# Kernel optimization log

Hardware: AMD Instinct MI355X
Metric: run time of the kernel (lower is better)

## Reference

```python
import jax, jax.numpy as jnp
import numpy as np

B, N, FIN, FOUT, E, R = 4, 8000, 256, 512, 640000, 44
NT = B * N
EPS = 1e-5


def setup_inputs() -> dict:
    key = jax.random.key(0)
    ks = jax.random.split(key, 10)
    s = 0.02
    return {
        "x": jax.random.normal(ks[0], (B, N, FIN), jnp.float32),
        "edge_index": jax.random.randint(ks[1], (2, E), 0, NT, jnp.int32),
        "edge_attr": jax.random.randint(ks[2], (E,), 0, R, jnp.int32),
        "gamma1": jnp.ones((FIN,), jnp.float32),
        "beta1": jnp.zeros((FIN,), jnp.float32),
        "W1": jax.random.normal(ks[3], (R, FIN, FOUT), jnp.float32) * s,
        "root1": jax.random.normal(ks[4], (FIN, FOUT), jnp.float32) * s,
        "b1": jnp.zeros((FOUT,), jnp.float32),
        "gamma2": jnp.ones((FOUT,), jnp.float32),
        "beta2": jnp.zeros((FOUT,), jnp.float32),
        "W2": jax.random.normal(ks[5], (R, FOUT, FOUT), jnp.float32) * s,
        "root2": jax.random.normal(ks[6], (FOUT, FOUT), jnp.float32) * s,
        "b2": jnp.zeros((FOUT,), jnp.float32),
        "Wskip": jax.random.normal(ks[7], (FIN, FOUT), jnp.float32) * s,
        "bskip": jnp.zeros((FOUT,), jnp.float32),
    }


def batchnorm(x, gamma, beta):
    # torch BatchNorm1d on (B, C, N) in training mode: stats over (B, N) per channel
    mu = jnp.mean(x, axis=(0, 1))
    var = jnp.var(x, axis=(0, 1))  # biased, matches torch normalization
    return (x - mu) * jax.lax.rsqrt(var + EPS) * gamma + beta


def rgcn_conv(h, src, dst, rel, W, root, bias):
    # out[i] = h[i]@root + bias + sum_r mean_{j in N_r(i)} h[j] @ W_r  (aggr='mean')
    n = h.shape[0]
    xs = h[src]  # [E, Fin] irregular gather
    # per-(node, relation) in-degree counts, computed once
    cnt = jnp.zeros((n, R), h.dtype).at[dst, rel].add(1.0)
    inv = 1.0 / jnp.maximum(cnt, 1.0)  # [n, R]
    out = h @ root + bias
    for r in range(R):  # static loop over relation types
        m = rel == r
        agg = jax.ops.segment_sum(jnp.where(m[:, None], xs, 0.0), dst, num_segments=n)
        out = out + (agg * inv[:, r:r + 1]) @ W[r]
    return out


def reference(x, edge_index, edge_attr, gamma1, beta1, W1, root1, b1,
              gamma2, beta2, W2, root2, b2, Wskip, bskip):
    src, dst = edge_index[0], edge_index[1]
    h = jax.nn.gelu(batchnorm(x, gamma1, beta1), approximate=False)
    hf = rgcn_conv(h.reshape(NT, FIN), src, dst, edge_attr, W1, root1, b1)
    h = jax.nn.gelu(batchnorm(hf.reshape(B, N, FOUT), gamma2, beta2), approximate=False)
    hf = rgcn_conv(h.reshape(NT, FOUT), src, dst, edge_attr, W2, root2, b2)
    skip = (x.reshape(NT, FIN) @ Wskip + bskip).reshape(B, N, FOUT)
    return hf.reshape(B, N, FOUT) + skip
```

## Files before the change

kernel.cpp:

```cpp
#include <hip/hip_runtime.h>
#include <cstdint>

#define E_NUM 640000
#define NTOT 32000
#define RNUM 44
#define NB (RNUM*NTOT)

typedef _Float16 f16x8 __attribute__((ext_vector_type(8)));
typedef _Float16 f16x4 __attribute__((ext_vector_type(4)));
typedef float    f32x4 __attribute__((ext_vector_type(4)));

__device__ __forceinline__ float gelu_f(float v) {
  return 0.5f * v * (1.0f + erff(v * 0.70710678118654752f));
}


__global__ void zero_int_k(int* __restrict__ p, int n) {
  int i = blockIdx.x * 256 + threadIdx.x;
  if (i < n) p[i] = 0;
}

__global__ void hist_k(const int* __restrict__ ei, const int* __restrict__ rel,
                       int* __restrict__ hist) {
  int e = blockIdx.x * 256 + threadIdx.x;
  if (e < E_NUM) {
    int d = ei[E_NUM + e];
    int r = rel[e];
    atomicAdd(&hist[r * NTOT + d], 1);
  }
}

__global__ void scan1_k(int* __restrict__ data, int* __restrict__ partials, int n) {
  __shared__ int ws[4];
  const int t = threadIdx.x;
  const int base = blockIdx.x * 1024 + t * 4;
  int v0 = 0, v1 = 0, v2 = 0, v3 = 0;
  if (base + 3 < n) {
    int4 u = *(const int4*)(data + base);
    v0 = u.x; v1 = u.y; v2 = u.z; v3 = u.w;
  } else if (base < n) {
    v0 = data[base];
    if (base + 1 < n) v1 = data[base + 1];
    if (base + 2 < n) v2 = data[base + 2];
  }
  const int tsum = v0 + v1 + v2 + v3;
  int incl = tsum;
  #pragma unroll
  for (int off = 1; off < 64; off <<= 1) {
    int u = __shfl_up(incl, off, 64);
    if ((t & 63) >= off) incl += u;
  }
  if ((t & 63) == 63) ws[t >> 6] = incl;
  __syncthreads();
  int wofs = 0;
  #pragma unroll
  for (int wv = 0; wv < 3; ++wv) if (wv < (t >> 6)) wofs += ws[wv];
  const int excl = wofs + incl - tsum;
  if (base + 3 < n) {
    int4 o; o.x = excl; o.y = excl + v0; o.z = excl + v0 + v1; o.w = excl + v0 + v1 + v2;
    *(int4*)(data + base) = o;
  } else if (base < n) {
    data[base] = excl;
    if (base + 1 < n) data[base + 1] = excl + v0;
    if (base + 2 < n) data[base + 2] = excl + v0 + v1;
  }
  if (t == 255) partials[blockIdx.x] = wofs + incl;
}

__global__ void scan2_k(int* __restrict__ p, int n) {
  __shared__ int ws[4];
  __shared__ int carryS;
  const int t = threadIdx.x;
  if (t == 0) carryS = 0;
  for (int chunk = 0; chunk < n; chunk += 1024) {
    __syncthreads();
    const int carry = carryS;
    const int base = chunk + t * 4;
    int v0 = 0, v1 = 0, v2 = 0, v3 = 0;
    if (base     < n) v0 = p[base];
    if (base + 1 < n) v1 = p[base + 1];
    if (base + 2 < n) v2 = p[base + 2];
    if (base + 3 < n) v3 = p[base + 3];
    const int tsum = v0 + v1 + v2 + v3;
    int incl = tsum;
    #pragma unroll
    for (int off = 1; off < 64; off <<= 1) {
      int u = __shfl_up(incl, off, 64);
      if ((t & 63) >= off) incl += u;
    }
    if ((t & 63) == 63) ws[t >> 6] = incl;
    __syncthreads();
    int wofs = 0;
    #pragma unroll
    for (int wv = 0; wv < 3; ++wv) if (wv < (t >> 6)) wofs += ws[wv];
    const int excl = carry + wofs + incl - tsum;
    if (base     < n) p[base]     = excl;
    if (base + 1 < n) p[base + 1] = excl + v0;
    if (base + 2 < n) p[base + 2] = excl + v0 + v1;
    if (base + 3 < n) p[base + 3] = excl + v0 + v1 + v2;
    __syncthreads();
    if (t == 255) carryS = carry + wofs + incl;
  }
}

__global__ void scan3_k(int* __restrict__ data, const int* __restrict__ partials, int n) {
  const int base = blockIdx.x * 1024 + threadIdx.x * 4;
  const int pofs = partials[blockIdx.x];
  if (base + 3 < n) {
    int4 u = *(const int4*)(data + base);
    u.x += pofs; u.y += pofs; u.z += pofs; u.w += pofs;
    *(int4*)(data + base) = u;
  } else if (base < n) {
    data[base] += pofs;
    if (base + 1 < n) data[base + 1] += pofs;
    if (base + 2 < n) data[base + 2] += pofs;
  }
}

__global__ void scatter_k(const int* __restrict__ ei, const int* __restrict__ rel,
                          int* __restrict__ cursor, int* __restrict__ sortedSrc) {
  int e = blockIdx.x * 256 + threadIdx.x;
  if (e < E_NUM) {
    int s = ei[e], d = ei[E_NUM + e], r = rel[e];
    int pos = atomicAdd(&cursor[r * NTOT + d], 1);
    sortedSrc[pos] = s;
  }
}


template<int C>
__global__ void bn_partial_k(const float* __restrict__ x, float* __restrict__ acc) {
  const int t = threadIdx.x;
  const int r0 = blockIdx.x * 128;
  constexpr int CC = C / 256;
  float s[CC], q[CC];
  #pragma unroll
  for (int cc = 0; cc < CC; ++cc) { s[cc] = 0.f; q[cc] = 0.f; }
  for (int r = 0; r < 128; ++r) {
    const float* row = x + (size_t)(r0 + r) * C + t;
    #pragma unroll
    for (int cc = 0; cc < CC; ++cc) { float v = row[cc * 256]; s[cc] += v; q[cc] += v * v; }
  }
  #pragma unroll
  for (int cc = 0; cc < CC; ++cc) {
    atomicAdd(&acc[t + cc * 256], s[cc]);
    atomicAdd(&acc[C + t + cc * 256], q[cc]);
  }
}

__global__ void bn_final_k(const float* __restrict__ acc, const float* __restrict__ gamma,
                           const float* __restrict__ beta, float* __restrict__ ss, int C) {
  int c = threadIdx.x;
  if (c < C) {
    float mean = acc[c] * (1.0f / 32000.0f);
    float var  = acc[C + c] * (1.0f / 32000.0f) - mean * mean;
    float sc = gamma[c] / sqrtf(var + 1e-5f);
    ss[c] = sc;
    ss[C + c] = beta[c] - mean * sc;
  }
}

__global__ void bn1_apply_k(const float* __restrict__ x, const float* __restrict__ ss,
                            _Float16* __restrict__ h16, _Float16* __restrict__ x16) {
  const int i = blockIdx.x * 256 + threadIdx.x;
  const float4 v = ((const float4*)x)[i];
  const int c4 = i & 63;
  const float4 sc = ((const float4*)ss)[c4];
  const float4 sh = ((const float4*)(ss + 256))[c4];
  f16x4 hv, xv;
  hv[0] = (_Float16)gelu_f(v.x * sc.x + sh.x);
  hv[1] = (_Float16)gelu_f(v.y * sc.y + sh.y);
  hv[2] = (_Float16)gelu_f(v.z * sc.z + sh.z);
  hv[3] = (_Float16)gelu_f(v.w * sc.w + sh.w);
  xv[0] = (_Float16)v.x; xv[1] = (_Float16)v.y; xv[2] = (_Float16)v.z; xv[3] = (_Float16)v.w;
  ((f16x4*)h16)[i] = hv;
  ((f16x4*)x16)[i] = xv;
}

__global__ void bn2_apply_k(const float* __restrict__ x, const float* __restrict__ ss,
                            _Float16* __restrict__ h16) {
  const int i = blockIdx.x * 256 + threadIdx.x;
  const float4 v = ((const float4*)x)[i];
  const int c4 = i & 127;
  const float4 sc = ((const float4*)ss)[c4];
  const float4 sh = ((const float4*)(ss + 512))[c4];
  f16x4 hv;
  hv[0] = (_Float16)gelu_f(v.x * sc.x + sh.x);
  hv[1] = (_Float16)gelu_f(v.y * sc.y + sh.y);
  hv[2] = (_Float16)gelu_f(v.z * sc.z + sh.z);
  hv[3] = (_Float16)gelu_f(v.w * sc.w + sh.w);
  ((f16x4*)h16)[i] = hv;
}

__global__ void prep_bt_k(const float* __restrict__ W, const float* __restrict__ root,
                          const float* __restrict__ skipw, int rkEnd, int rootEnd, int Kfull,
                          _Float16* __restrict__ Bt) {
  __shared__ float tile[64][72];
  const int kb = blockIdx.x * 64, nb = blockIdx.y * 64;
  const int t = threadIdx.x;
  {
    const int i = t >> 2, j = (t & 3) * 16;
    const int kk = kb + i;
    const float* srow = (kk < rkEnd) ? (W + (size_t)kk * 512)
                      : ((kk < rootEnd) ? (root + (size_t)(kk - rkEnd) * 512)
                                        : (skipw + (size_t)(kk - rootEnd) * 512));
    #pragma unroll
    for (int q2 = 0; q2 < 4; ++q2) {
      float4 v = *(const float4*)(srow + nb + j + q2 * 4);
      *(float4*)&tile[i][j + q2 * 4] = v;
    }
  }
  __syncthreads();
  {
    const int nl = t >> 2, kg = (t & 3) * 16;
    const int n = nb + nl;
    const int s = (n & 7) << 3;
    #pragma unroll
    for (int g = 0; g < 2; ++g) {
      const int d0 = kg + g * 8;
      const int j0 = d0 ^ s;
      f16x8 o;
      #pragma unroll
      for (int u = 0; u < 8; ++u) o[u] = (_Float16)tile[j0 + u][nl];
      *(f16x8*)(Bt + (size_t)n * Kfull + kb + d0) = o;
    }
  }
}

template<int KH, int KSTEPS, int RK, int ROOTEND, bool HAS_SKIP>
__global__ __launch_bounds__(512, 4) void gemm_fused_k(
    const _Float16* __restrict__ h16, const _Float16* __restrict__ x16,
    const _Float16* __restrict__ Bt, const int* __restrict__ keyOff,
    const int* __restrict__ sortedSrc, const float* __restrict__ biasA,
    const float* __restrict__ biasB, float* __restrict__ out)
{
  constexpr int KFULL = HAS_SKIP ? (ROOTEND + 256) : ROOTEND;
  constexpr int LOG2KH = (KH == 256) ? 8 : 9;
  __shared__ _Float16 Alds[64 * 64];
  __shared__ _Float16 Blds[512 * 64];
  const int tid = threadIdx.x;
  const int lane = tid & 63;
  const int w = tid >> 6;
  const int wr = w >> 2, wc = w & 3;
  const int m0 = blockIdx.x * 64;
  const int arow = tid >> 3;
  const int tsub = tid & 7;
  const int tcol = tsub * 8;
  const int gi = m0 + arow;

  f32x4 acc[2][8];
  #pragma unroll
  for (int m = 0; m < 2; ++m)
    #pragma unroll
    for (int n = 0; n < 8; ++n)
      acc[m][n] = f32x4{0.f, 0.f, 0.f, 0.f};

  int off0 = 0, cnt = 0;
  int c0 = 0, c1 = 0, c2 = 0;
  float inv = 0.f;

  char* const aldsrow = (char*)Alds + arow * 128;
  const int swz = (arow & 7) << 4;

  for (int kt = 0; kt < KSTEPS; ++kt) {
    const int k0 = kt * 64;
    {
      const _Float16* gB = Bt + (size_t)(w * 64 + (lane >> 3)) * KFULL + k0 + (lane & 7) * 8;
      #pragma unroll
      for (int q = 0; q < 8; ++q) {
        __builtin_amdgcn_global_load_lds(
            (const __attribute__((address_space(1))) void*)(gB + (size_t)q * 8 * KFULL),
            (__attribute__((address_space(3))) void*)(Blds + (w * 64 + q * 8) * 64),
            16, 0, 0);
      }
    }
    if (k0 < RK) {
      const int klocal = k0 & (KH - 1);
      if (klocal == 0) {
        const int r = k0 >> LOG2KH;
        const int bin = r * NTOT + gi;
        off0 = keyOff[bin];
        const int o1 = keyOff[bin + 1];
        cnt = o1 - off0;
        inv = (cnt > 0) ? (1.0f / (float)cnt) : 0.0f;
        if (cnt > 0) c0 = sortedSrc[off0];
        if (cnt > 1) c1 = sortedSrc[off0 + 1];
        if (cnt > 2) c2 = sortedSrc[off0 + 2];
      }
      if (cnt == 0) {
        *(f16x8*)(aldsrow + ((tcol * 2) ^ swz)) = f16x8{};
      } else {
        f16x8 a0, a1, a2;
        a0 = *(const f16x8*)(h16 + (size_t)c0 * KH + klocal + tcol);
        if (cnt > 1) a1 = *(const f16x8*)(h16 + (size_t)c1 * KH + klocal + tcol);
        if (cnt > 2) a2 = *(const f16x8*)(h16 + (size_t)c2 * KH + klocal + tcol);
        float sacc[8];
        #pragma unroll
        for (int j = 0; j < 8; ++j) sacc[j] = (float)a0[j];
        if (cnt > 1) {
          #pragma unroll
          for (int j = 0; j < 8; ++j) sacc[j] += (float)a1[j];
        }
        if (cnt > 2) {
          #pragma unroll
          for (int j = 0; j < 8; ++j) sacc[j] += (float)a2[j];
        }
        for (int e = off0 + 3; e < off0 + cnt; ++e) {
          const int s = sortedSrc[e];
          const f16x8 av = *(const f16x8*)(h16 + (size_t)s * KH + klocal + tcol);
          #pragma unroll
          for (int j = 0; j < 8; ++j) sacc[j] += (float)av[j];
        }
        f16x8 o;
        #pragma unroll
        for (int j = 0; j < 8; ++j) o[j] = (_Float16)(sacc[j] * inv);
        *(f16x8*)(aldsrow + ((tcol * 2) ^ swz)) = o;
      }
    } else {
      const _Float16* sp;
      if (!HAS_SKIP || k0 < ROOTEND) sp = h16 + (size_t)gi * KH + (k0 - RK);
      else                           sp = x16 + (size_t)gi * 256 + (k0 - ROOTEND);
      const f16x8 v = *(const f16x8*)(sp + tcol);
      *(f16x8*)(aldsrow + ((tcol * 2) ^ swz)) = v;
    }
    __syncthreads();
    #pragma unroll
    for (int kh2 = 0; kh2 < 2; ++kh2) {
      const int kByte = kh2 * 64 + ((lane >> 4) << 4);
      f16x8 af[2];
      #pragma unroll
      for (int m = 0; m < 2; ++m) {
        const int row = wr * 32 + m * 16 + (lane & 15);
        af[m] = *(const f16x8*)((const char*)Alds + row * 128 + (kByte ^ ((row & 7) << 4)));
      }
      #pragma unroll
      for (int n = 0; n < 8; ++n) {
        const int col = wc * 128 + n * 16 + (lane & 15);
        const f16x8 bf = *(const f16x8*)((const char*)Blds + col * 128 + (kByte ^ ((col & 7) << 4)));
        #pragma unroll
        for (int m = 0; m < 2; ++m)
          acc[m][n] = __builtin_amdgcn_mfma_f32_16x16x32_f16(af[m], bf, acc[m][n], 0, 0, 0);
      }
    }
    __syncthreads();
  }
  #pragma unroll
  for (int m = 0; m < 2; ++m) {
    const int grow = m0 + wr * 32 + m * 16 + ((lane >> 4) << 2);
    #pragma unroll
    for (int n = 0; n < 8; ++n) {
      const int gcol = wc * 128 + n * 16 + (lane & 15);
      float badd = biasA[gcol];
      if (HAS_SKIP) badd += biasB[gcol];
      #pragma unroll
      for (int q = 0; q < 4; ++q) {
        out[(size_t)(grow + q) * 512 + gcol] = acc[m][n][q] + badd;
      }
    }
  }
}


extern "C" void kernel_launch(void* const* d_in, const int* in_sizes, int n_in,
                              void* d_out, int out_size, void* d_ws, size_t ws_size,
                              hipStream_t stream) {
  const float* x      = (const float*)d_in[0];
  const int*   ei     = (const int*)d_in[1];
  const int*   rel    = (const int*)d_in[2];
  const float* gamma1 = (const float*)d_in[3];
  const float* beta1  = (const float*)d_in[4];
  const float* W1     = (const float*)d_in[5];
  const float* root1  = (const float*)d_in[6];
  const float* b1     = (const float*)d_in[7];
  const float* gamma2 = (const float*)d_in[8];
  const float* beta2  = (const float*)d_in[9];
  const float* W2     = (const float*)d_in[10];
  const float* root2  = (const float*)d_in[11];
  const float* b2     = (const float*)d_in[12];
  const float* Wskip  = (const float*)d_in[13];
  const float* bskip  = (const float*)d_in[14];
  float* out = (float*)d_out;

  uintptr_t p = (uintptr_t)d_ws;
  auto carve = [&](size_t bytes) -> void* {
    void* r = (void*)p;
    p += (bytes + 255) & ~(size_t)255;
    return r;
  };
  int*      keyOff    = (int*)carve((size_t)(NB + 8) * 4);
  int*      cursor    = (int*)carve((size_t)(NB + 8) * 4);
  int*      partials  = (int*)carve(2048 * 4);
  int*      sortedSrc = (int*)carve((size_t)E_NUM * 4);
  float*    bnAcc1    = (float*)carve(512 * 4);
  float*    bnAcc2    = (float*)carve(1024 * 4);
  float*    ss1       = (float*)carve(512 * 4);
  float*    ss2       = (float*)carve(1024 * 4);
  _Float16* Bt1       = (_Float16*)carve((size_t)512 * 11520 * 2);
  _Float16* Bt2       = (_Float16*)carve((size_t)512 * 23296 * 2);
  _Float16* x16       = (_Float16*)carve((size_t)NTOT * 256 * 2);
  _Float16* h16       = (_Float16*)carve((size_t)NTOT * 512 * 2);
  float*    out1      = (float*)carve((size_t)NTOT * 512 * 4);

  zero_int_k<<<(NB + 1 + 255) / 256, 256, 0, stream>>>(keyOff, NB + 1);
  zero_int_k<<<6, 256, 0, stream>>>((int*)bnAcc1, 1536);

  prep_bt_k<<<dim3(180, 8), 256, 0, stream>>>(W1, root1, root1, 11264, 11520, 11520, Bt1);
  prep_bt_k<<<dim3(364, 8), 256, 0, stream>>>(W2, root2, Wskip, 22528, 23040, 23296, Bt2);

  bn_partial_k<256><<<250, 256, 0, stream>>>(x, bnAcc1);
  bn_final_k<<<1, 256, 0, stream>>>(bnAcc1, gamma1, beta1, ss1, 256);
  bn1_apply_k<<<8000, 256, 0, stream>>>(x, ss1, h16, x16);

  hist_k<<<2500, 256, 0, stream>>>(ei, rel, keyOff);
  scan1_k<<<1376, 256, 0, stream>>>(keyOff, partials, NB + 1);
  scan2_k<<<1, 256, 0, stream>>>(partials, 1376);
  scan3_k<<<1376, 256, 0, stream>>>(keyOff, partials, NB + 1);
  hipMemcpyAsync(cursor, keyOff, (size_t)NB * 4, hipMemcpyDeviceToDevice, stream);
  scatter_k<<<2500, 256, 0, stream>>>(ei, rel, cursor, sortedSrc);

  gemm_fused_k<256, 180, 11264, 11520, false><<<500, 512, 0, stream>>>(
      h16, x16, Bt1, keyOff, sortedSrc, b1, b1, out1);

  bn_partial_k<512><<<250, 256, 0, stream>>>(out1, bnAcc2);
  bn_final_k<<<1, 512, 0, stream>>>(bnAcc2, gamma2, beta2, ss2, 512);
  bn2_apply_k<<<16000, 256, 0, stream>>>(out1, ss2, h16);

  gemm_fused_k<512, 364, 22528, 23040, true><<<500, 512, 0, stream>>>(
      h16, x16, Bt2, keyOff, sortedSrc, b2, bskip, out);
}
```

Measured before the change: 1.736 ms.

## Double-buffer B tiles, prefetch A gathers, and double the M tile to 128 rows

The fused gather+GEMM kernel now processes 128 rows per block instead of 64. Each thread gathers 16 halfs per row, and each wave computes a 64x128 output tile. B tiles are double-buffered in LDS: the next k-step's B and the first three gathered neighbor rows are loaded while MFMAs run on the current step. The grid halves to 250 blocks, which on a 256-CU device leaves some CUs idle. More LDS (about 144KB) and registers per block cut occupancy to one or two blocks per CU.

```diff
diff --git a/kernel.cpp b/kernel.cpp
--- a/kernel.cpp
+++ b/kernel.cpp
@@ -228,7 +228,7 @@
 }
 
 template<int KH, int KSTEPS, int RK, int ROOTEND, bool HAS_SKIP>
-__global__ __launch_bounds__(512, 4) void gemm_fused_k(
+__global__ __launch_bounds__(512, 2) void gemm_fused_k(
     const _Float16* __restrict__ h16, const _Float16* __restrict__ x16,
     const _Float16* __restrict__ Bt, const int* __restrict__ keyOff,
     const int* __restrict__ sortedSrc, const float* __restrict__ biasA,
@@ -236,47 +236,39 @@
 {
   constexpr int KFULL = HAS_SKIP ? (ROOTEND + 256) : ROOTEND;
   constexpr int LOG2KH = (KH == 256) ? 8 : 9;
-  __shared__ _Float16 Alds[64 * 64];
-  __shared__ _Float16 Blds[512 * 64];
+  __shared__ _Float16 Alds[128 * 64];
+  __shared__ _Float16 Blds[2 * 512 * 64];
   const int tid = threadIdx.x;
   const int lane = tid & 63;
   const int w = tid >> 6;
   const int wr = w >> 2, wc = w & 3;
-  const int m0 = blockIdx.x * 64;
-  const int arow = tid >> 3;
-  const int tsub = tid & 7;
-  const int tcol = tsub * 8;
+  const int m0 = blockIdx.x * 128;
+  const int arow = tid >> 2;
+  const int tsub = tid & 3;
+  const int tcol = tsub * 16;
   const int gi = m0 + arow;
 
-  f32x4 acc[2][8];
-  #pragma unroll
-  for (int m = 0; m < 2; ++m)
+  f32x4 acc[4][8];
+  #pragma unroll
+  for (int m = 0; m < 4; ++m)
     #pragma unroll
     for (int n = 0; n < 8; ++n)
       acc[m][n] = f32x4{0.f, 0.f, 0.f, 0.f};
 
-  int off0 = 0, cnt = 0;
+  char* const aldsrow = (char*)Alds + arow * 128;
+  const int swz = (arow & 7) << 4;
+
+  int off0 = 0, cnt = 0, klcur = 0;
   int c0 = 0, c1 = 0, c2 = 0;
   float inv = 0.f;
-
-  char* const aldsrow = (char*)Alds + arow * 128;
-  const int swz = (arow & 7) << 4;
-
-  for (int kt = 0; kt < KSTEPS; ++kt) {
+  f16x8 g0a{}, g0b{}, g1a{}, g1b{}, g2a{}, g2b{};
+
+  auto prefetch = [&](int kt) {
     const int k0 = kt * 64;
-    {
-      const _Float16* gB = Bt + (size_t)(w * 64 + (lane >> 3)) * KFULL + k0 + (lane & 7) * 8;
-      #pragma unroll
-      for (int q = 0; q < 8; ++q) {
-        __builtin_amdgcn_global_load_lds(
-            (const __attribute__((address_space(1))) void*)(gB + (size_t)q * 8 * KFULL),
-            (__attribute__((address_space(3))) void*)(Blds + (w * 64 + q * 8) * 64),
-            16, 0, 0);
-      }
-    }
     if (k0 < RK) {
-      const int klocal = k0 & (KH - 1);
-      if (klocal == 0) {
+      const int kl = k0 & (KH - 1);
+      klcur = kl;
+      if (kl == 0) {
         const int r = k0 >> LOG2KH;
         const int bin = r * NTOT + gi;
         off0 = keyOff[bin];
@@ -287,66 +279,111 @@
         if (cnt > 1) c1 = sortedSrc[off0 + 1];
         if (cnt > 2) c2 = sortedSrc[off0 + 2];
       }
-      if (cnt == 0) {
-        *(f16x8*)(aldsrow + ((tcol * 2) ^ swz)) = f16x8{};
-      } else {
-        f16x8 a0, a1, a2;
-        a0 = *(const f16x8*)(h16 + (size_t)c0 * KH + klocal + tcol);
-        if (cnt > 1) a1 = *(const f16x8*)(h16 + (size_t)c1 * KH + klocal + tcol);
-        if (cnt > 2) a2 = *(const f16x8*)(h16 + (size_t)c2 * KH + klocal + tcol);
-        float sacc[8];
-        #pragma unroll
-        for (int j = 0; j < 8; ++j) sacc[j] = (float)a0[j];
+      if (cnt > 0) {
+        const _Float16* p0 = h16 + (size_t)c0 * KH + kl + tcol;
+        g0a = *(const f16x8*)p0;  g0b = *(const f16x8*)(p0 + 8);
         if (cnt > 1) {
-          #pragma unroll
-          for (int j = 0; j < 8; ++j) sacc[j] += (float)a1[j];
+          const _Float16* p1 = h16 + (size_t)c1 * KH + kl + tcol;
+          g1a = *(const f16x8*)p1;  g1b = *(const f16x8*)(p1 + 8);
         }
         if (cnt > 2) {
-          #pragma unroll
-          for (int j = 0; j < 8; ++j) sacc[j] += (float)a2[j];
+          const _Float16* p2 = h16 + (size_t)c2 * KH + kl + tcol;
+          g2a = *(const f16x8*)p2;  g2b = *(const f16x8*)(p2 + 8);
         }
-        for (int e = off0 + 3; e < off0 + cnt; ++e) {
-          const int s = sortedSrc[e];
-          const f16x8 av = *(const f16x8*)(h16 + (size_t)s * KH + klocal + tcol);
-          #pragma unroll
-          for (int j = 0; j < 8; ++j) sacc[j] += (float)av[j];
-        }
-        f16x8 o;
-        #pragma unroll
-        for (int j = 0; j < 8; ++j) o[j] = (_Float16)(sacc[j] * inv);
-        *(f16x8*)(aldsrow + ((tcol * 2) ^ swz)) = o;
       }
     } else {
       const _Float16* sp;
       if (!HAS_SKIP || k0 < ROOTEND) sp = h16 + (size_t)gi * KH + (k0 - RK);
       else                           sp = x16 + (size_t)gi * 256 + (k0 - ROOTEND);
-      const f16x8 v = *(const f16x8*)(sp + tcol);
-      *(f16x8*)(aldsrow + ((tcol * 2) ^ swz)) = v;
-    }
+      cnt = 1; inv = 1.0f;
+      g0a = *(const f16x8*)(sp + tcol);
+      g0b = *(const f16x8*)(sp + tcol + 8);
+    }
+  };
+
+  auto write_a = [&]() {
+    if (cnt == 0) {
+      *(f16x8*)(aldsrow + ((tcol * 2) ^ swz)) = f16x8{};
+      *(f16x8*)(aldsrow + ((tcol * 2 + 16) ^ swz)) = f16x8{};
+    } else {
+      float sa[16];
+      #pragma unroll
+      for (int j = 0; j < 8; ++j) { sa[j] = (float)g0a[j]; sa[8 + j] = (float)g0b[j]; }
+      if (cnt > 1) {
+        #pragma unroll
+        for (int j = 0; j < 8; ++j) { sa[j] += (float)g1a[j]; sa[8 + j] += (float)g1b[j]; }
+      }
+      if (cnt > 2) {
+        #pragma unroll
+        for (int j = 0; j < 8; ++j) { sa[j] += (float)g2a[j]; sa[8 + j] += (float)g2b[j]; }
+      }
+      for (int e = off0 + 3; e < off0 + cnt; ++e) {
+        const int s = sortedSrc[e];
+        const _Float16* hp = h16 + (size_t)s * KH + klcur + tcol;
+        const f16x8 va = *(const f16x8*)hp;
+        const f16x8 vb = *(const f16x8*)(hp + 8);
+        #pragma unroll
+        for (int j = 0; j < 8; ++j) { sa[j] += (float)va[j]; sa[8 + j] += (float)vb[j]; }
+      }
+      f16x8 o0, o1;
+      #pragma unroll
+      for (int j = 0; j < 8; ++j) {
+        o0[j] = (_Float16)(sa[j] * inv);
+        o1[j] = (_Float16)(sa[8 + j] * inv);
+      }
+      *(f16x8*)(aldsrow + ((tcol * 2) ^ swz)) = o0;
+      *(f16x8*)(aldsrow + ((tcol * 2 + 16) ^ swz)) = o1;
+    }
+  };
+
+  auto stage_b = [&](int kt, int bufsel) {
+    const int k0 = kt * 64;
+    const _Float16* gB = Bt + (size_t)(w * 64 + (lane >> 3)) * KFULL + k0 + (lane & 7) * 8;
+    _Float16* bb = Blds + (size_t)bufsel * (512 * 64);
+    #pragma unroll
+    for (int q = 0; q < 8; ++q) {
+      __builtin_amdgcn_global_load_lds(
+          (const __attribute__((address_space(1))) void*)(gB + (size_t)q * 8 * KFULL),
+          (__attribute__((address_space(3))) void*)(bb + (w * 64 + q * 8) * 64),
+          16, 0, 0);
+    }
+  };
+
+  prefetch(0);
+  stage_b(0, 0);
+
+  for (int kt = 0; kt < KSTEPS; ++kt) {
+    const int cur = kt & 1;
+    write_a();
     __syncthreads();
+    if (kt + 1 < KSTEPS) {
+      prefetch(kt + 1);
+      stage_b(kt + 1, cur ^ 1);
+    }
+    const char* bbase = (const char*)(Blds + (size_t)cur * (512 * 64));
     #pragma unroll
     for (int kh2 = 0; kh2 < 2; ++kh2) {
       const int kByte = kh2 * 64 + ((lane >> 4) << 4);
-      f16x8 af[2];
-      #pragma unroll
-      for (int m = 0; m < 2; ++m) {
-        const int row = wr * 32 + m * 16 + (lane & 15);
+      f16x8 af[4];
+      #pragma unroll
+      for (int m = 0; m < 4; ++m) {
+        const int row = wr * 64 + m * 16 + (lane & 15);
         af[m] = *(const f16x8*)((const char*)Alds + row * 128 + (kByte ^ ((row & 7) << 4)));
       }
       #pragma unroll
       for (int n = 0; n < 8; ++n) {
         const int col = wc * 128 + n * 16 + (lane & 15);
-        const f16x8 bf = *(const f16x8*)((const char*)Blds + col * 128 + (kByte ^ ((col & 7) << 4)));
+        const f16x8 bf = *(const f16x8*)(bbase + col * 128 + (kByte ^ ((col & 7) << 4)));
         #pragma unroll
-        for (int m = 0; m < 2; ++m)
+        for (int m = 0; m < 4; ++m)
           acc[m][n] = __builtin_amdgcn_mfma_f32_16x16x32_f16(af[m], bf, acc[m][n], 0, 0, 0);
       }
     }
     __syncthreads();
   }
   #pragma unroll
-  for (int m = 0; m < 2; ++m) {
-    const int grow = m0 + wr * 32 + m * 16 + ((lane >> 4) << 2);
+  for (int m = 0; m < 4; ++m) {
+    const int grow = m0 + wr * 64 + m * 16 + ((lane >> 4) << 2);
     #pragma unroll
     for (int n = 0; n < 8; ++n) {
       const int gcol = wc * 128 + n * 16 + (lane & 15);
@@ -418,13 +455,13 @@
   hipMemcpyAsync(cursor, keyOff, (size_t)NB * 4, hipMemcpyDeviceToDevice, stream);
   scatter_k<<<2500, 256, 0, stream>>>(ei, rel, cursor, sortedSrc);
 
-  gemm_fused_k<256, 180, 11264, 11520, false><<<500, 512, 0, stream>>>(
+  gemm_fused_k<256, 180, 11264, 11520, false><<<250, 512, 0, stream>>>(
       h16, x16, Bt1, keyOff, sortedSrc, b1, b1, out1);
 
   bn_partial_k<512><<<250, 256, 0, stream>>>(out1, bnAcc2);
   bn_final_k<<<1, 512, 0, stream>>>(bnAcc2, gamma2, beta2, ss2, 512);
   bn2_apply_k<<<16000, 256, 0, stream>>>(out1, ss2, h16);
 
-  gemm_fused_k<512, 364, 22528, 23040, true><<<500, 512, 0, stream>>>(
+  gemm_fused_k<512, 364, 22528, 23040, true><<<250, 512, 0, stream>>>(
       h16, x16, Bt2, keyOff, sortedSrc, b2, bskip, out);
 }
```

After: 1.953 ms. 1.13x slower.

## Retile fused RGCN GEMM to 128x256 blocks with XCD-aware block remapping

Applied to the files above, without the earlier changes.

Changes the fused gather+GEMM block tile from 64 rows x 512 cols to 128 rows x 256 cols. Each block now gathers and averages 128 node rows per k-step, 16 halves per thread. Each wave computes a 64x64 sub-tile with a 4x4 MFMA accumulator grid, which raises A-fragment reuse and halves the B tile staged per block. Block IDs are remapped per XCD so the two column halves of the same rows land close together, and s_setprio is raised around the MFMA section. In exchange, the irregular neighbour gather is now done twice per row, once per column half, which doubles that gather traffic.

```diff
diff --git a/kernel.cpp b/kernel.cpp
--- a/kernel.cpp
+++ b/kernel.cpp
@@ -236,23 +236,27 @@
 {
   constexpr int KFULL = HAS_SKIP ? (ROOTEND + 256) : ROOTEND;
   constexpr int LOG2KH = (KH == 256) ? 8 : 9;
-  __shared__ _Float16 Alds[64 * 64];
-  __shared__ _Float16 Blds[512 * 64];
+  __shared__ _Float16 Alds[128 * 64];
+  __shared__ _Float16 Blds[256 * 64];
   const int tid = threadIdx.x;
   const int lane = tid & 63;
   const int w = tid >> 6;
   const int wr = w >> 2, wc = w & 3;
-  const int m0 = blockIdx.x * 64;
-  const int arow = tid >> 3;
-  const int tsub = tid & 7;
-  const int tcol = tsub * 8;
+  const int raw = blockIdx.x;
+  const int xcd = raw & 7, idx = raw >> 3;
+  const int wg = (xcd < 4) ? (xcd * 63 + idx) : (252 + (xcd - 4) * 62 + idx);
+  const int n0 = (wg & 1) << 8;
+  const int m0 = (wg >> 1) << 7;
+  const int arow = tid >> 2;
+  const int tsub = tid & 3;
+  const int tcol = tsub * 16;
   const int gi = m0 + arow;
 
-  f32x4 acc[2][8];
-  #pragma unroll
-  for (int m = 0; m < 2; ++m)
-    #pragma unroll
-    for (int n = 0; n < 8; ++n)
+  f32x4 acc[4][4];
+  #pragma unroll
+  for (int m = 0; m < 4; ++m)
+    #pragma unroll
+    for (int n = 0; n < 4; ++n)
       acc[m][n] = f32x4{0.f, 0.f, 0.f, 0.f};
 
   int off0 = 0, cnt = 0;
@@ -265,12 +269,12 @@
   for (int kt = 0; kt < KSTEPS; ++kt) {
     const int k0 = kt * 64;
     {
-      const _Float16* gB = Bt + (size_t)(w * 64 + (lane >> 3)) * KFULL + k0 + (lane & 7) * 8;
+      const _Float16* gB = Bt + (size_t)(n0 + w * 32 + (lane >> 3)) * KFULL + k0 + (lane & 7) * 8;
       #pragma unroll
-      for (int q = 0; q < 8; ++q) {
+      for (int q = 0; q < 4; ++q) {
         __builtin_amdgcn_global_load_lds(
             (const __attribute__((address_space(1))) void*)(gB + (size_t)q * 8 * KFULL),
-            (__attribute__((address_space(3))) void*)(Blds + (w * 64 + q * 8) * 64),
+            (__attribute__((address_space(3))) void*)(Blds + (w * 32 + q * 8) * 64),
             16, 0, 0);
       }
     }
@@ -289,67 +293,83 @@
       }
       if (cnt == 0) {
         *(f16x8*)(aldsrow + ((tcol * 2) ^ swz)) = f16x8{};
+        *(f16x8*)(aldsrow + ((tcol * 2 + 16) ^ swz)) = f16x8{};
       } else {
-        f16x8 a0, a1, a2;
-        a0 = *(const f16x8*)(h16 + (size_t)c0 * KH + klocal + tcol);
-        if (cnt > 1) a1 = *(const f16x8*)(h16 + (size_t)c1 * KH + klocal + tcol);
-        if (cnt > 2) a2 = *(const f16x8*)(h16 + (size_t)c2 * KH + klocal + tcol);
-        float sacc[8];
+        const _Float16* p0 = h16 + (size_t)c0 * KH + klocal + tcol;
+        const f16x8 a0a = *(const f16x8*)p0;
+        const f16x8 a0b = *(const f16x8*)(p0 + 8);
+        float sa[16];
         #pragma unroll
-        for (int j = 0; j < 8; ++j) sacc[j] = (float)a0[j];
+        for (int j = 0; j < 8; ++j) { sa[j] = (float)a0a[j]; sa[8 + j] = (float)a0b[j]; }
         if (cnt > 1) {
+          const _Float16* p1 = h16 + (size_t)c1 * KH + klocal + tcol;
+          const f16x8 a1a = *(const f16x8*)p1;
+          const f16x8 a1b = *(const f16x8*)(p1 + 8);
           #pragma unroll
-          for (int j = 0; j < 8; ++j) sacc[j] += (float)a1[j];
+          for (int j = 0; j < 8; ++j) { sa[j] += (float)a1a[j]; sa[8 + j] += (float)a1b[j]; }
         }
         if (cnt > 2) {
+          const _Float16* p2 = h16 + (size_t)c2 * KH + klocal + tcol;
+          const f16x8 a2a = *(const f16x8*)p2;
+          const f16x8 a2b = *(const f16x8*)(p2 + 8);
           #pragma unroll
-          for (int j = 0; j < 8; ++j) sacc[j] += (float)a2[j];
+          for (int j = 0; j < 8; ++j) { sa[j] += (float)a2a[j]; sa[8 + j] += (float)a2b[j]; }
         }
         for (int e = off0 + 3; e < off0 + cnt; ++e) {
           const int s = sortedSrc[e];
-          const f16x8 av = *(const f16x8*)(h16 + (size_t)s * KH + klocal + tcol);
+          const _Float16* hp = h16 + (size_t)s * KH + klocal + tcol;
+          const f16x8 va = *(const f16x8*)hp;
+          const f16x8 vb = *(const f16x8*)(hp + 8);
           #pragma unroll
-          for (int j = 0; j < 8; ++j) sacc[j] += (float)av[j];
+          for (int j = 0; j < 8; ++j) { sa[j] += (float)va[j]; sa[8 + j] += (float)vb[j]; }
         }
-        f16x8 o;
+        f16x8 o0, o1;
         #pragma unroll
-        for (int j = 0; j < 8; ++j) o[j] = (_Float16)(sacc[j] * inv);
-        *(f16x8*)(aldsrow + ((tcol * 2) ^ swz)) = o;
+        for (int j = 0; j < 8; ++j) {
+          o0[j] = (_Float16)(sa[j] * inv);
+          o1[j] = (_Float16)(sa[8 + j] * inv);
+        }
+        *(f16x8*)(aldsrow + ((tcol * 2) ^ swz)) = o0;
+        *(f16x8*)(aldsrow + ((tcol * 2 + 16) ^ swz)) = o1;
       }
     } else {
       const _Float16* sp;
       if (!HAS_SKIP || k0 < ROOTEND) sp = h16 + (size_t)gi * KH + (k0 - RK);
       else                           sp = x16 + (size_t)gi * 256 + (k0 - ROOTEND);
-      const f16x8 v = *(const f16x8*)(sp + tcol);
-      *(f16x8*)(aldsrow + ((tcol * 2) ^ swz)) = v;
+      const f16x8 v0 = *(const f16x8*)(sp + tcol);
+      const f16x8 v1 = *(const f16x8*)(sp + tcol + 8);
+      *(f16x8*)(aldsrow + ((tcol * 2) ^ swz)) = v0;
+      *(f16x8*)(aldsrow + ((tcol * 2 + 16) ^ swz)) = v1;
     }
     __syncthreads();
+    __builtin_amdgcn_s_setprio(1);
     #pragma unroll
     for (int kh2 = 0; kh2 < 2; ++kh2) {
       const int kByte = kh2 * 64 + ((lane >> 4) << 4);
-      f16x8 af[2];
+      f16x8 af[4];
       #pragma unroll
-      for (int m = 0; m < 2; ++m) {
-        const int row = wr * 32 + m * 16 + (lane & 15);
+      for (int m = 0; m < 4; ++m) {
+        const int row = wr * 64 + m * 16 + (lane & 15);
         af[m] = *(const f16x8*)((const char*)Alds + row * 128 + (kByte ^ ((row & 7) << 4)));
       }
       #pragma unroll
-      for (int n = 0; n < 8; ++n) {
-        const int col = wc * 128 + n * 16 + (lane & 15);
+      for (int n = 0; n < 4; ++n) {
+        const int col = wc * 64 + n * 16 + (lane & 15);
         const f16x8 bf = *(const f16x8*)((const char*)Blds + col * 128 + (kByte ^ ((col & 7) << 4)));
         #pragma unroll
-        for (int m = 0; m < 2; ++m)
+        for (int m = 0; m < 4; ++m)
           acc[m][n] = __builtin_amdgcn_mfma_f32_16x16x32_f16(af[m], bf, acc[m][n], 0, 0, 0);
       }
     }
+    __builtin_amdgcn_s_setprio(0);
     __syncthreads();
   }
   #pragma unroll
-  for (int m = 0; m < 2; ++m) {
-    const int grow = m0 + wr * 32 + m * 16 + ((lane >> 4) << 2);
-    #pragma unroll
-    for (int n = 0; n < 8; ++n) {
-      const int gcol = wc * 128 + n * 16 + (lane & 15);
+  for (int m = 0; m < 4; ++m) {
+    const int grow = m0 + wr * 64 + m * 16 + ((lane >> 4) << 2);
+    #pragma unroll
+    for (int n = 0; n < 4; ++n) {
+      const int gcol = n0 + wc * 64 + n * 16 + (lane & 15);
       float badd = biasA[gcol];
       if (HAS_SKIP) badd += biasB[gcol];
       #pragma unroll
```

New measurement: 1.951 ms. 1.12x slower.

## Software-pipeline gather and B loads in fused RGCN GEMM, remap warp tiles

Applied to the files above, without the earlier changes.

Restructures the fused gather+GEMM main loop so the gathered neighbor rows for the next k-step and the B tile loads are issued one step ahead, with explicit vmcnt waits and raw s_barriers instead of __syncthreads. This is meant to hide the latency of the irregular h16 gathers and keyOff/sortedSrc lookups behind MFMA work. Each warp now covers all 64 rows and a 64-column slice (4x4 accumulators) instead of a 32x128 tile, which changes how much LDS traffic goes to A versus B fragments. It also reads the first three source indices with one int4 load and always loads three rows, padding sortedSrc so that read stays in bounds. The hand-counted waitcnts could go wrong if the compiler reorders memory operations.

```diff
diff --git a/kernel.cpp b/kernel.cpp
--- a/kernel.cpp
+++ b/kernel.cpp
@@ -241,115 +241,165 @@
   const int tid = threadIdx.x;
   const int lane = tid & 63;
   const int w = tid >> 6;
-  const int wr = w >> 2, wc = w & 3;
   const int m0 = blockIdx.x * 64;
   const int arow = tid >> 3;
   const int tsub = tid & 7;
   const int tcol = tsub * 8;
   const int gi = m0 + arow;
 
-  f32x4 acc[2][8];
-  #pragma unroll
-  for (int m = 0; m < 2; ++m)
-    #pragma unroll
-    for (int n = 0; n < 8; ++n)
+  f32x4 acc[4][4];
+  #pragma unroll
+  for (int m = 0; m < 4; ++m)
+    #pragma unroll
+    for (int n = 0; n < 4; ++n)
       acc[m][n] = f32x4{0.f, 0.f, 0.f, 0.f};
+
+  char* const aldsrow = (char*)Alds + arow * 128;
+  const int swz = (arow & 7) << 4;
 
   int off0 = 0, cnt = 0;
   int c0 = 0, c1 = 0, c2 = 0;
   float inv = 0.f;
-
-  char* const aldsrow = (char*)Alds + arow * 128;
-  const int swz = (arow & 7) << 4;
+  int2 koPre{0, 0};
+  f16x8 g0{}, g1{}, g2{};
+
+  auto issueB = [&](int kt) {
+    const int k0 = kt * 64;
+    const _Float16* gB = Bt + (size_t)(w * 64 + (lane >> 3)) * KFULL + k0 + (lane & 7) * 8;
+    #pragma unroll
+    for (int q = 0; q < 8; ++q) {
+      __builtin_amdgcn_global_load_lds(
+          (const __attribute__((address_space(1))) void*)(gB + (size_t)q * 8 * KFULL),
+          (__attribute__((address_space(3))) void*)(Blds + (w * 64 + q * 8) * 64),
+          16, 0, 0);
+    }
+  };
+
+  auto gatherChain = [&]() {
+    off0 = koPre.x;
+    cnt = koPre.y - koPre.x;
+    inv = (cnt > 0) ? (1.0f / (float)cnt) : 0.0f;
+    if (cnt > 0) {
+      const int4 cs = *(const int4*)(sortedSrc + off0);
+      c0 = cs.x;
+      c1 = (cnt > 1) ? cs.y : cs.x;
+      c2 = (cnt > 2) ? cs.z : cs.x;
+    } else { c0 = 0; c1 = 0; c2 = 0; }
+    g0 = *(const f16x8*)(h16 + (size_t)c0 * KH + tcol);
+    g1 = *(const f16x8*)(h16 + (size_t)c1 * KH + tcol);
+    g2 = *(const f16x8*)(h16 + (size_t)c2 * KH + tcol);
+  };
+
+  auto writeA = [&](int klocal) {
+    float sa[8];
+    #pragma unroll
+    for (int j = 0; j < 8; ++j) sa[j] = (float)g0[j];
+    if (cnt > 1) {
+      #pragma unroll
+      for (int j = 0; j < 8; ++j) sa[j] += (float)g1[j];
+    }
+    if (cnt > 2) {
+      #pragma unroll
+      for (int j = 0; j < 8; ++j) sa[j] += (float)g2[j];
+    }
+    for (int e = off0 + 3; e < off0 + cnt; ++e) {
+      const int s = sortedSrc[e];
+      const f16x8 v = *(const f16x8*)(h16 + (size_t)s * KH + klocal + tcol);
+      #pragma unroll
+      for (int j = 0; j < 8; ++j) sa[j] += (float)v[j];
+    }
+    f16x8 o;
+    #pragma unroll
+    for (int j = 0; j < 8; ++j) o[j] = (_Float16)(sa[j] * inv);
+    *(f16x8*)(aldsrow + ((tcol * 2) ^ swz)) = o;
+  };
+
+  auto prefetchFor = [&](int k) {
+    if (k >= KSTEPS) return;
+    const int k0 = k * 64;
+    if (k0 >= RK) {
+      const _Float16* sp = (!HAS_SKIP || k0 < ROOTEND)
+          ? (h16 + (size_t)gi * KH + (k0 - RK))
+          : (x16 + (size_t)gi * 256 + (k0 - ROOTEND));
+      g0 = *(const f16x8*)(sp + tcol);
+    } else if ((k0 & (KH - 1)) == 0) {
+      koPre = *(const int2*)(keyOff + (size_t)(k0 >> LOG2KH) * NTOT + gi);
+    } else {
+      const _Float16* base = h16 + (k0 & (KH - 1)) + tcol;
+      g0 = *(const f16x8*)(base + (size_t)c0 * KH);
+      g1 = *(const f16x8*)(base + (size_t)c1 * KH);
+      g2 = *(const f16x8*)(base + (size_t)c2 * KH);
+    }
+  };
+
+  auto waitSel = [&](int k) {
+    int nsel;
+    if (k >= KSTEPS) nsel = 0;
+    else {
+      const int k0 = k * 64;
+      if (k0 >= RK) nsel = 1;
+      else if ((k0 & (KH - 1)) == 0) nsel = 1;
+      else nsel = 3;
+    }
+    if (nsel == 3)      asm volatile("s_waitcnt vmcnt(3) lgkmcnt(0)" ::: "memory");
+    else if (nsel == 1) asm volatile("s_waitcnt vmcnt(1) lgkmcnt(0)" ::: "memory");
+    else                asm volatile("s_waitcnt vmcnt(0) lgkmcnt(0)" ::: "memory");
+  };
+
+  issueB(0);
+  koPre = *(const int2*)(keyOff + gi);
+  gatherChain();
+  writeA(0);
+  prefetchFor(1);
+  waitSel(1);
+  __builtin_amdgcn_sched_barrier(0);
+  __builtin_amdgcn_s_barrier();
+  __builtin_amdgcn_sched_barrier(0);
 
   for (int kt = 0; kt < KSTEPS; ++kt) {
-    const int k0 = kt * 64;
-    {
-      const _Float16* gB = Bt + (size_t)(w * 64 + (lane >> 3)) * KFULL + k0 + (lane & 7) * 8;
-      #pragma unroll
-      for (int q = 0; q < 8; ++q) {
-        __builtin_amdgcn_global_load_lds(
-            (const __attribute__((address_space(1))) void*)(gB + (size_t)q * 8 * KFULL),
-            (__attribute__((address_space(3))) void*)(Blds + (w * 64 + q * 8) * 64),
-            16, 0, 0);
-      }
-    }
-    if (k0 < RK) {
-      const int klocal = k0 & (KH - 1);
-      if (klocal == 0) {
-        const int r = k0 >> LOG2KH;
-        const int bin = r * NTOT + gi;
-        off0 = keyOff[bin];
-        const int o1 = keyOff[bin + 1];
-        cnt = o1 - off0;
-        inv = (cnt > 0) ? (1.0f / (float)cnt) : 0.0f;
-        if (cnt > 0) c0 = sortedSrc[off0];
-        if (cnt > 1) c1 = sortedSrc[off0 + 1];
-        if (cnt > 2) c2 = sortedSrc[off0 + 2];
-      }
-      if (cnt == 0) {
-        *(f16x8*)(aldsrow + ((tcol * 2) ^ swz)) = f16x8{};
-      } else {
-        f16x8 a0, a1, a2;
-        a0 = *(const f16x8*)(h16 + (size_t)c0 * KH + klocal + tcol);
-        if (cnt > 1) a1 = *(const f16x8*)(h16 + (size_t)c1 * KH + klocal + tcol);
-        if (cnt > 2) a2 = *(const f16x8*)(h16 + (size_t)c2 * KH + klocal + tcol);
-        float sacc[8];
-        #pragma unroll
-        for (int j = 0; j < 8; ++j) sacc[j] = (float)a0[j];
-        if (cnt > 1) {
-          #pragma unroll
-          for (int j = 0; j < 8; ++j) sacc[j] += (float)a1[j];
-        }
-        if (cnt > 2) {
-          #pragma unroll
-          for (int j = 0; j < 8; ++j) sacc[j] += (float)a2[j];
-        }
-        for (int e = off0 + 3; e < off0 + cnt; ++e) {
-          const int s = sortedSrc[e];
-          const f16x8 av = *(const f16x8*)(h16 + (size_t)s * KH + klocal + tcol);
-          #pragma unroll
-          for (int j = 0; j < 8; ++j) sacc[j] += (float)av[j];
-        }
-        f16x8 o;
-        #pragma unroll
-        for (int j = 0; j < 8; ++j) o[j] = (_Float16)(sacc[j] * inv);
-        *(f16x8*)(aldsrow + ((tcol * 2) ^ swz)) = o;
-      }
-    } else {
-      const _Float16* sp;
-      if (!HAS_SKIP || k0 < ROOTEND) sp = h16 + (size_t)gi * KH + (k0 - RK);
-      else                           sp = x16 + (size_t)gi * 256 + (k0 - ROOTEND);
-      const f16x8 v = *(const f16x8*)(sp + tcol);
-      *(f16x8*)(aldsrow + ((tcol * 2) ^ swz)) = v;
-    }
-    __syncthreads();
     #pragma unroll
     for (int kh2 = 0; kh2 < 2; ++kh2) {
       const int kByte = kh2 * 64 + ((lane >> 4) << 4);
-      f16x8 af[2];
-      #pragma unroll
-      for (int m = 0; m < 2; ++m) {
-        const int row = wr * 32 + m * 16 + (lane & 15);
+      f16x8 af[4];
+      #pragma unroll
+      for (int m = 0; m < 4; ++m) {
+        const int row = m * 16 + (lane & 15);
         af[m] = *(const f16x8*)((const char*)Alds + row * 128 + (kByte ^ ((row & 7) << 4)));
       }
       #pragma unroll
-      for (int n = 0; n < 8; ++n) {
-        const int col = wc * 128 + n * 16 + (lane & 15);
+      for (int n = 0; n < 4; ++n) {
+        const int col = w * 64 + n * 16 + (lane & 15);
         const f16x8 bf = *(const f16x8*)((const char*)Blds + col * 128 + (kByte ^ ((col & 7) << 4)));
         #pragma unroll
-        for (int m = 0; m < 2; ++m)
+        for (int m = 0; m < 4; ++m)
           acc[m][n] = __builtin_amdgcn_mfma_f32_16x16x32_f16(af[m], bf, acc[m][n], 0, 0, 0);
       }
     }
-    __syncthreads();
-  }
-  #pragma unroll
-  for (int m = 0; m < 2; ++m) {
-    const int grow = m0 + wr * 32 + m * 16 + ((lane >> 4) << 2);
-    #pragma unroll
-    for (int n = 0; n < 8; ++n) {
-      const int gcol = wc * 128 + n * 16 + (lane & 15);
+    __builtin_amdgcn_sched_barrier(0);
+    __builtin_amdgcn_s_barrier();
+    __builtin_amdgcn_sched_barrier(0);
+    if (kt + 1 < KSTEPS) {
+      const int k0n = (kt + 1) * 64;
+      issueB(kt + 1);
+      if (k0n < RK) {
+        if ((k0n & (KH - 1)) == 0) { gatherChain(); writeA(0); }
+        else                       writeA(k0n & (KH - 1));
+      } else {
+        *(f16x8*)(aldsrow + ((tcol * 2) ^ swz)) = g0;
+      }
+      prefetchFor(kt + 2);
+      waitSel(kt + 2);
+      __builtin_amdgcn_sched_barrier(0);
+      __builtin_amdgcn_s_barrier();
+      __builtin_amdgcn_sched_barrier(0);
+    }
+  }
+  #pragma unroll
+  for (int m = 0; m < 4; ++m) {
+    const int grow = m0 + m * 16 + ((lane >> 4) << 2);
+    #pragma unroll
+    for (int n = 0; n < 4; ++n) {
+      const int gcol = w * 64 + n * 16 + (lane & 15);
       float badd = biasA[gcol];
       if (HAS_SKIP) badd += biasB[gcol];
       #pragma unroll
@@ -390,7 +440,7 @@
   int*      keyOff    = (int*)carve((size_t)(NB + 8) * 4);
   int*      cursor    = (int*)carve((size_t)(NB + 8) * 4);
   int*      partials  = (int*)carve(2048 * 4);
-  int*      sortedSrc = (int*)carve((size_t)E_NUM * 4);
+  int*      sortedSrc = (int*)carve((size_t)(E_NUM + 8) * 4);
   float*    bnAcc1    = (float*)carve(512 * 4);
   float*    bnAcc2    = (float*)carve(1024 * 4);
   float*    ss1       = (float*)carve(512 * 4);
```

Result: slower. 1.867 ms (+7.6%).
